# Performance work log

Measured on AMD Instinct MI355X. Metric: run time of the kernel, lower is better.

Reference implementation:

```python
import math
import jax, jax.numpy as jnp
import numpy as np

D_MODEL = 1024
N_HEADS = 16
D_K = D_MODEL // N_HEADS
THETA = 10000.0


def setup_inputs() -> dict:
    key = jax.random.key(0)
    k1, k2, k3 = jax.random.split(key, 3)
    B, S = 2, 2048
    x = jax.random.normal(k1, (B, S, D_MODEL), dtype=jnp.float32)
    std_qkv = math.sqrt(2.0 / (D_MODEL + 3 * D_MODEL))
    std_out = math.sqrt(2.0 / (D_MODEL + D_MODEL))
    # Linear weights stored as (out_features, in_features) to match the
    # einsum '... i, o i -> ... o' contraction (trunc-normal approximated
    # by clipped normal for the reference baseline).
    w_qkv = jnp.clip(jax.random.normal(k2, (3 * D_MODEL, D_MODEL), dtype=jnp.float32) * std_qkv,
                     -3 * std_qkv, 3 * std_qkv)
    b_qkv = jnp.zeros((3 * D_MODEL,), dtype=jnp.float32)
    w_out = jnp.clip(jax.random.normal(k3, (D_MODEL, D_MODEL), dtype=jnp.float32) * std_out,
                     -3 * std_out, 3 * std_out)
    b_out = jnp.zeros((D_MODEL,), dtype=jnp.float32)
    return {"x": x, "w_qkv": w_qkv, "b_qkv": b_qkv, "w_out": w_out, "b_out": b_out}


def _rope(t, cos, sin):
    # t: (B, H, S, D_K); cos/sin: (S, D_K//2) broadcast over batch/heads.
    B, H, S, d = t.shape
    tp = t.reshape(B, H, S, d // 2, 2)
    even, odd = tp[..., 0], tp[..., 1]
    r_even = even * cos - odd * sin
    r_odd = even * sin + odd * cos
    return jnp.stack([r_even, r_odd], axis=-1).reshape(B, H, S, d)


def reference(x, w_qkv, b_qkv, w_out, b_out):
    B, S, _ = x.shape
    # QKV projection: weight is (out, in)
    qkv = jnp.einsum('bsi,oi->bso', x, w_qkv) + b_qkv  # (B, S, 3*D_MODEL)
    qkv = qkv.reshape(B, S, 3, N_HEADS, D_K).transpose(2, 0, 3, 1, 4)  # (3, B, H, S, D_K)
    q, k, v = qkv[0], qkv[1], qkv[2]

    # RoPE with default token_positions = arange(S)
    inv_freq = THETA ** (-(jnp.arange(0, D_K, 2, dtype=jnp.float32)) / D_K)  # (D_K//2,)
    ang = jnp.arange(S, dtype=jnp.float32)[:, None] * inv_freq[None, :]      # (S, D_K//2)
    cos, sin = jnp.cos(ang), jnp.sin(ang)
    q = _rope(q, cos, sin)
    k = _rope(k, cos, sin)

    # Scaled dot-product attention in fp32 with causal mask
    scale = 1.0 / math.sqrt(D_K)
    scores = jnp.einsum('bhqd,bhkd->bhqk', q.astype(jnp.float32), k.astype(jnp.float32)) * scale
    causal = jnp.tril(jnp.ones((S, S), dtype=bool))
    scores = jnp.where(causal, scores, jnp.finfo(jnp.float32).min)
    # Custom softmax: exp(x - max) / (sum + 1e-8)
    ex = jnp.exp(scores - jnp.max(scores, axis=-1, keepdims=True))
    attn = ex / (jnp.sum(ex, axis=-1, keepdims=True) + 1e-8)
    attn = attn.astype(v.dtype)

    o = jnp.einsum('bhqk,bhkd->bhqd', attn, v)           # (B, H, S, D_K)
    o = o.transpose(0, 2, 1, 3).reshape(B, S, D_MODEL)    # (B, S, D_MODEL)
    out = jnp.einsum('bsi,oi->bso', o, w_out) + b_out
    return out
```

## Files before the change

kernel.cpp:

```cpp
#include <hip/hip_runtime.h>


typedef float f32x4 __attribute__((ext_vector_type(4)));
typedef float fvec4 __attribute__((ext_vector_type(4)));
typedef __bf16 bf16x8 __attribute__((ext_vector_type(8)));
typedef unsigned int u32x4 __attribute__((ext_vector_type(4)));

#define S_SZ 2048
#define NH 16
#define DK 64

static __device__ __forceinline__ unsigned short f2bf(float f) {
  unsigned int u = __builtin_bit_cast(unsigned int, f);
  u += 0x7fffu + ((u >> 16) & 1u);
  return (unsigned short)(u >> 16);
}
static __device__ __forceinline__ float bf2f(unsigned short h) {
  unsigned int u = ((unsigned int)h) << 16;
  return __builtin_bit_cast(float, u);
}
static __device__ __forceinline__ unsigned int pk2(float a, float b) {
  return (unsigned int)f2bf(a) | ((unsigned int)f2bf(b) << 16);
}
static __device__ __forceinline__ bf16x8 ld16g(const unsigned short* p) {
  return __builtin_bit_cast(bf16x8, *(const u32x4*)p);
}
static __device__ __forceinline__ void gload_lds16(const unsigned short* g,
                                                   unsigned short* l) {
  __builtin_amdgcn_global_load_lds(
      (const __attribute__((address_space(1))) void*)g,
      (__attribute__((address_space(3))) void*)l, 16, 0, 0);
}
static __device__ __forceinline__ float ex2(float x) {
  float r;
  asm("v_exp_f32 %0, %1" : "=v"(r) : "v"(x));
  return r;
}
static __device__ __forceinline__ unsigned int cvtpk(float a, float b) {
  unsigned int r;
  asm("v_cvt_pk_bf16_f32 %0, %1, %2" : "=v"(r) : "v"(a), "v"(b));
  return r;
}

template <int CTRL>
static __device__ __forceinline__ float dppmov(float x) {
  return __builtin_bit_cast(
      float, __builtin_amdgcn_update_dpp(0, __builtin_bit_cast(int, x), CTRL,
                                         0xF, 0xF, true));
}
static __device__ __forceinline__ float rmax16(float x) {
  x = fmaxf(x, dppmov<0xB1>(x));
  x = fmaxf(x, dppmov<0x4E>(x));
  x = fmaxf(x, dppmov<0x141>(x));
  x = fmaxf(x, dppmov<0x140>(x));
  return x;
}
static __device__ __forceinline__ float rsum16(float x) {
  x += dppmov<0xB1>(x);
  x += dppmov<0x4E>(x);
  x += dppmov<0x141>(x);
  x += dppmov<0x140>(x);
  return x;
}

__global__ __launch_bounds__(256) void cvt_bf16(
    const float* __restrict__ x, const float* __restrict__ wq,
    const float* __restrict__ wo, unsigned short* __restrict__ xb,
    unsigned short* __restrict__ wqb, unsigned short* __restrict__ wob) {
  const int u = blockIdx.x * 256 + threadIdx.x;
  const float* src;
  unsigned short* dst;
  int idx;
  if (u < 524288) { src = x; dst = xb; idx = u; }
  else if (u < 917504) { src = wq; dst = wqb; idx = u - 524288; }
  else { src = wo; dst = wob; idx = u - 917504; }
  const fvec4* p = (const fvec4*)(src + (size_t)idx * 8);
  const fvec4 f0 = p[0], f1 = p[1];
  u32x4 o;
  o[0] = pk2(f0[0], f0[1]); o[1] = pk2(f0[2], f0[3]);
  o[2] = pk2(f1[0], f1[1]); o[3] = pk2(f1[2], f1[3]);
  *(u32x4*)(dst + (size_t)idx * 8) = o;
}

template <bool OBF16>
__global__ __launch_bounds__(256) void gemm_bf16(
    const unsigned short* __restrict__ A, const unsigned short* __restrict__ B,
    const float* __restrict__ bias, void* __restrict__ Cp, int N, int K) {
  __shared__ unsigned short As[2][4096];
  __shared__ unsigned short Bs[2][4096];
  const int t = threadIdx.x;
  const int lane = t & 63, w = t >> 6;
  const int lo = lane & 15, g = lane >> 4;
  const int wr = (w >> 1) * 64, wc = (w & 1) * 64;
  const int gx = gridDim.x;
  int o = blockIdx.y * gx + blockIdx.x;
  const int nwg = gx * gridDim.y;
  o = (o & 7) * (nwg >> 3) + (o >> 3);
  const int by = o / gx, bx = o - by * gx;
  const int bRow = by * 128, bCol = bx * 128;
  const unsigned short* ap = A + (size_t)(bRow + (t >> 2)) * K + (t & 3) * 8;
  const unsigned short* bp = B + (size_t)(bCol + (t >> 2)) * K + (t & 3) * 8;
  const size_t rK = (size_t)64 * K;
  const int wb = w * 512;
  f32x4 acc[4][4] = {};
  gload_lds16(ap, As[0] + wb);
  gload_lds16(ap + rK, As[0] + 2048 + wb);
  gload_lds16(bp, Bs[0] + wb);
  gload_lds16(bp + rK, Bs[0] + 2048 + wb);
  const int nk = K >> 5;
  for (int kt = 0; kt < nk; ++kt) {
    __syncthreads();
    if (kt + 1 < nk) {
      const int k0 = (kt + 1) << 5;
      const int nb = (kt + 1) & 1;
      gload_lds16(ap + k0, As[nb] + wb);
      gload_lds16(ap + rK + k0, As[nb] + 2048 + wb);
      gload_lds16(bp + k0, Bs[nb] + wb);
      gload_lds16(bp + rK + k0, Bs[nb] + 2048 + wb);
    }
    const unsigned short* Ac = As[kt & 1];
    const unsigned short* Bc = Bs[kt & 1];
    bf16x8 aF[4], bF[4];
#pragma unroll
    for (int m = 0; m < 4; ++m) aF[m] = ld16g(Ac + (wr + m * 16 + lo) * 32 + 8 * g);
#pragma unroll
    for (int n = 0; n < 4; ++n) bF[n] = ld16g(Bc + (wc + n * 16 + lo) * 32 + 8 * g);
    __builtin_amdgcn_s_setprio(1);
#pragma unroll
    for (int m = 0; m < 4; ++m)
#pragma unroll
      for (int n = 0; n < 4; ++n)
        acc[m][n] = __builtin_amdgcn_mfma_f32_16x16x32_bf16(aF[m], bF[n], acc[m][n], 0, 0, 0);
    __builtin_amdgcn_s_setprio(0);
  }
#pragma unroll
  for (int m = 0; m < 4; ++m) {
#pragma unroll
    for (int n = 0; n < 4; ++n) {
      const int col = bCol + wc + n * 16 + lo;
      const float bv = bias[col];
#pragma unroll
      for (int r = 0; r < 4; ++r) {
        const int row = bRow + wr + m * 16 + g * 4 + r;
        const float v = acc[m][n][r] + bv;
        if constexpr (OBF16)
          ((unsigned short*)Cp)[(size_t)row * N + col] = f2bf(v);
        else
          ((float*)Cp)[(size_t)row * N + col] = v;
      }
    }
  }
}

__global__ __launch_bounds__(256) void rope_scatter(
    const unsigned short* __restrict__ qkv, unsigned short* __restrict__ Qo,
    unsigned short* __restrict__ Ko, unsigned short* __restrict__ Vt) {
  const int t = blockIdx.x * 256 + threadIdx.x;
  const int i = t & 31;
  const int s = (t >> 5) & (S_SZ - 1);
  const int h = (t >> 16) & (NH - 1);
  const int b = t >> 20;
  const unsigned short* row = qkv + (size_t)(b * S_SZ + s) * 3072;
  const float inv = exp2f((float)i * (-13.287712379549449f / 32.0f));
  const float ang = (float)s * inv;
  float sn, cs;
  sincosf(ang, &sn, &cs);
  const unsigned int qp = *(const unsigned int*)(row + h * 64 + 2 * i);
  const unsigned int kp = *(const unsigned int*)(row + 1024 + h * 64 + 2 * i);
  const unsigned int vp = *(const unsigned int*)(row + 2048 + h * 64 + 2 * i);
  const float qe = bf2f((unsigned short)qp), qo = bf2f((unsigned short)(qp >> 16));
  const float ke = bf2f((unsigned short)kp), ko = bf2f((unsigned short)(kp >> 16));
  const size_t hb = (size_t)(b * NH + h);
  const size_t qkbase = (hb * S_SZ + s) * DK + 2 * i;
  const float qs = 0.18033688011112042f;
  *(unsigned int*)(Qo + qkbase) =
      pk2((qe * cs - qo * sn) * qs, (qe * sn + qo * cs) * qs);
  *(unsigned int*)(Ko + qkbase) = pk2(ke * cs - ko * sn, ke * sn + ko * cs);
  const size_t vb = (hb * DK + 2 * i) * S_SZ + s;
  Vt[vb] = (unsigned short)vp;
  Vt[vb + S_SZ] = (unsigned short)(vp >> 16);
}

static __device__ __forceinline__ void stage8(const unsigned short* __restrict__ gbase,
                                              int gstride, unsigned short* tile, int t) {
  const int r = t >> 3;
  const int s16 = (t & 7) ^ (r & 7);
  gload_lds16(gbase + (size_t)r * gstride + (s16 << 3), tile + (t >> 6) * 512);
}

static __device__ __forceinline__ void attn_step(
    const unsigned short* __restrict__ Kl, const unsigned short* __restrict__ Vl,
    unsigned short* __restrict__ Pw, const bf16x8 aQ0, const bf16x8 aQ1,
    const bool diag, const int wq, const int lo, const int g,
    float* __restrict__ m, float* __restrict__ lsum, f32x4* __restrict__ oacc) {
  f32x4 s[4];
  __builtin_amdgcn_s_setprio(1);
#pragma unroll
  for (int c = 0; c < 4; ++c) {
    const int kr = c * 16 + lo;
    const int sw = kr & 7;
    const bf16x8 b0 =
        __builtin_bit_cast(bf16x8, *(const u32x4*)&Kl[kr * 64 + ((g ^ sw) << 3)]);
    const bf16x8 b1 =
        __builtin_bit_cast(bf16x8, *(const u32x4*)&Kl[kr * 64 + (((4 + g) ^ sw) << 3)]);
    f32x4 z = {};
    z = __builtin_amdgcn_mfma_f32_16x16x32_bf16(aQ0, b0, z, 0, 0, 0);
    z = __builtin_amdgcn_mfma_f32_16x16x32_bf16(aQ1, b1, z, 0, 0, 0);
    s[c] = z;
  }
  __builtin_amdgcn_s_setprio(0);
  if (diag) {
#pragma unroll
    for (int c = 0; c < 4; ++c)
#pragma unroll
      for (int r = 0; r < 4; ++r)
        if ((c * 16 + lo) > (wq * 16 + g * 4 + r)) s[c][r] = -__builtin_inff();
  }
  float rm[4];
#pragma unroll
  for (int r = 0; r < 4; ++r) {
    const float v = fmaxf(fmaxf(s[0][r], s[1][r]), fmaxf(s[2][r], s[3][r]));
    rm[r] = rmax16(v);
  }
  const bool grow = (rm[0] > m[0] + 8.f) | (rm[1] > m[1] + 8.f) |
                    (rm[2] > m[2] + 8.f) | (rm[3] > m[3] + 8.f);
  if (__any((int)grow)) {
#pragma unroll
    for (int r = 0; r < 4; ++r) {
      const float mn = fmaxf(m[r], rm[r]);
      const float alpha = ex2(m[r] - mn);
      m[r] = mn;
      lsum[r] *= alpha;
#pragma unroll
      for (int nt = 0; nt < 4; ++nt) oacc[nt][r] *= alpha;
    }
  }
#pragma unroll
  for (int r = 0; r < 4; ++r) {
    float rs = 0.f;
#pragma unroll
    for (int c = 0; c < 4; ++c) {
      const float p = ex2(s[c][r] - m[r]);
      s[c][r] = p;
      rs += p;
    }
    lsum[r] += rsum16(rs);
    const unsigned int u01 = cvtpk(s[0][r], s[1][r]);
    const unsigned int u23 = cvtpk(s[2][r], s[3][r]);
    unsigned short* pr = Pw + (g * 4 + r) * 72 + lo;
    pr[0] = (unsigned short)u01;
    pr[16] = (unsigned short)(u01 >> 16);
    pr[32] = (unsigned short)u23;
    pr[48] = (unsigned short)(u23 >> 16);
  }
  __builtin_amdgcn_s_setprio(1);
#pragma unroll
  for (int kc = 0; kc < 2; ++kc) {
    const bf16x8 aP =
        __builtin_bit_cast(bf16x8, *(const u32x4*)&Pw[lo * 72 + kc * 32 + 8 * g]);
#pragma unroll
    for (int nt = 0; nt < 4; ++nt) {
      const int d = nt * 16 + lo;
      const bf16x8 bV = __builtin_bit_cast(
          bf16x8, *(const u32x4*)&Vl[d * 64 + (((kc * 4 + g) ^ (d & 7)) << 3)]);
      oacc[nt] = __builtin_amdgcn_mfma_f32_16x16x32_bf16(aP, bV, oacc[nt], 0, 0, 0);
    }
  }
  __builtin_amdgcn_s_setprio(0);
}

__global__ __launch_bounds__(512, 2) void flash_attn(
    const unsigned short* __restrict__ Q, const unsigned short* __restrict__ K,
    const unsigned short* __restrict__ VT, unsigned short* __restrict__ O) {
  __shared__ unsigned short Kb[4][4096];
  __shared__ unsigned short Vb[4][4096];
  __shared__ unsigned short Pl[8][1152];
  const int t = threadIdx.x;
  const int lane = t & 63, w = t >> 6;
  const int lo = lane & 15, g = lane >> 4;
  const int flat = blockIdx.y * 16 + blockIdx.x;
  const int bh = ((flat & 7) << 2) | ((flat >> 3) & 3);
  const int j = flat >> 5;
  const int qa = j, qb = 31 - j;
  const unsigned short* Qh = Q + (size_t)bh * S_SZ * DK;
  const unsigned short* Kh = K + (size_t)bh * S_SZ * DK;
  const unsigned short* Vh = VT + (size_t)bh * DK * S_SZ;

  const int wq = w & 3;
  const bool s1 = w >= 4;
  const int rowMain = (s1 ? qb : qa) * 64 + wq * 16;
  const int rowB = qb * 64 + wq * 16;
  const bf16x8 aQ0 = ld16g(Qh + (size_t)(rowMain + lo) * DK + 8 * g);
  const bf16x8 aQ1 = ld16g(Qh + (size_t)(rowMain + lo) * DK + 32 + 8 * g);
  bf16x8 aQB0 = aQ0, aQB1 = aQ1;
  if (!s1) {
    aQB0 = ld16g(Qh + (size_t)(rowB + lo) * DK + 8 * g);
    aQB1 = ld16g(Qh + (size_t)(rowB + lo) * DK + 32 + 8 * g);
  }

  float mA[4], lA[4], mB[4], lB[4];
  f32x4 oA[4] = {}, oB[4] = {};
#pragma unroll
  for (int r = 0; r < 4; ++r) {
    mA[r] = mB[r] = -__builtin_inff();
    lA[r] = lB[r] = 0.f;
  }
  unsigned short* Pw = &Pl[w][0];

  stage8(Kh, DK, Kb[0], t);
  stage8(Vh, S_SZ, Vb[0], t);
  __syncthreads();
  for (int i = 0; i <= 16; ++i) {
    if (i < 15) {
      stage8(Kh + (size_t)(i + 1) * 64 * DK, DK, Kb[(i + 1) & 1], t);
      stage8(Vh + (i + 1) * 64, S_SZ, Vb[(i + 1) & 1], t);
    }
    if (i >= qa && i <= 15) {
      const int tile = 16 + (i - qa);
      stage8(Kh + (size_t)tile * 64 * DK, DK, Kb[2 + ((i - qa) & 1)], t);
      stage8(Vh + tile * 64, S_SZ, Vb[2 + ((i - qa) & 1)], t);
    }
    if (s1) {
      if (i < 16) {
        attn_step(Kb[i & 1], Vb[i & 1], Pw, aQ0, aQ1, false, wq, lo, g, mA, lA, oA);
      } else {
        float* ml = (float*)Pw;
#pragma unroll
        for (int r = 0; r < 4; ++r) {
          ml[r * 64 + lane] = mA[r];
          ml[(4 + r) * 64 + lane] = lA[r];
        }
        float* obase = (w < 6) ? ((float*)&Kb[1][0]) + (w - 4) * 1024
                               : ((float*)&Vb[1][0]) + (w - 6) * 1024;
#pragma unroll
        for (int nt = 0; nt < 4; ++nt)
#pragma unroll
          for (int r = 0; r < 4; ++r) obase[(nt * 4 + r) * 64 + lane] = oA[nt][r];
      }
    } else {
      if (i <= qa) {
        attn_step(Kb[i & 1], Vb[i & 1], Pw, aQ0, aQ1, i == qa, wq, lo, g, mA, lA, oA);
      } else {
        const int d = i - qa - 1;
        attn_step(Kb[2 + (d & 1)], Vb[2 + (d & 1)], Pw, aQB0, aQB1, i == 16, wq,
                  lo, g, mB, lB, oB);
      }
    }
    __syncthreads();
  }

  if (!s1) {
    const int b = bh >> 4, h = bh & 15;
#pragma unroll
    for (int r = 0; r < 4; ++r) {
      const float inv = 1.0f / (lA[r] + 1e-8f);
      const size_t base = ((size_t)(b * S_SZ + rowMain + g * 4 + r)) * 1024 + h * DK;
#pragma unroll
      for (int nt = 0; nt < 4; ++nt) O[base + nt * 16 + lo] = f2bf(oA[nt][r] * inv);
    }
    const float* ml = (const float*)&Pl[w + 4][0];
    const float* obase = (w < 2) ? ((const float*)&Kb[1][0]) + w * 1024
                                 : ((const float*)&Vb[1][0]) + (w - 2) * 1024;
#pragma unroll
    for (int r = 0; r < 4; ++r) {
      const float m1 = ml[r * 64 + lane], l1 = ml[(4 + r) * 64 + lane];
      const float mh = fmaxf(mB[r], m1);
      const float a0 = ex2(mB[r] - mh), a1 = ex2(m1 - mh);
      const float linv = 1.0f / (lB[r] * a0 + l1 * a1 + 1e-8f);
      const size_t base = ((size_t)(b * S_SZ + rowB + g * 4 + r)) * 1024 + h * DK;
#pragma unroll
      for (int nt = 0; nt < 4; ++nt)
        O[base + nt * 16 + lo] =
            f2bf((oB[nt][r] * a0 + obase[(nt * 4 + r) * 64 + lane] * a1) * linv);
    }
  }
}

extern "C" void kernel_launch(void* const* d_in, const int* in_sizes, int n_in,
                              void* d_out, int out_size, void* d_ws, size_t ws_size,
                              hipStream_t stream) {
  const float* x = (const float*)d_in[0];
  const float* w_qkv = (const float*)d_in[1];
  const float* b_qkv = (const float*)d_in[2];
  const float* w_out = (const float*)d_in[3];
  const float* b_out = (const float*)d_in[4];
  float* out = (float*)d_out;

  char* ws = (char*)d_ws;
  unsigned short* xb = (unsigned short*)(ws);
  unsigned short* wqb = (unsigned short*)(ws + 8388608);
  unsigned short* wob = (unsigned short*)(ws + 14680064);
  unsigned short* qkv = (unsigned short*)(ws + 16777216);
  unsigned short* kb = (unsigned short*)(ws + 41943040);
  unsigned short* vt = (unsigned short*)(ws + 50331648);
  unsigned short* qb = xb;
  unsigned short* ob = qkv;

  cvt_bf16<<<4096, 256, 0, stream>>>(x, w_qkv, w_out, xb, wqb, wob);
  {
    dim3 grid(3072 / 128, 4096 / 128);
    gemm_bf16<true><<<grid, 256, 0, stream>>>(xb, wqb, b_qkv, qkv, 3072, 1024);
  }
  rope_scatter<<<(2 * NH * S_SZ * 32) / 256, 256, 0, stream>>>(qkv, qb, kb, vt);
  {
    dim3 grid(16, 2 * NH);
    flash_attn<<<grid, 512, 0, stream>>>(qb, kb, vt, ob);
  }
  {
    dim3 grid(1024 / 128, 4096 / 128);
    gemm_bf16<false><<<grid, 256, 0, stream>>>(ob, wob, b_out, out, 1024, 1024);
  }
}
```

Measured before the change: 140.6 us.

## Read second-stream V directly from global memory and shrink LDS for higher occupancy

Drops the LDS staging buffers for the second query tile's V and has that path load V operands straight from global memory. It also repacks the per-wave P scratch from padded 72-stride rows into XOR-swizzled 64-stride rows. Together these cut shared memory use, and launch bounds are raised from 2 to 4 blocks per CU. The trade-off is uncached, uncoalesced-ish global loads inside the MFMA loop and possible register pressure at the higher occupancy target. The end-of-loop merge still writes into Vb[1], which the smaller buffer keeps.

```diff
diff --git a/kernel.cpp b/kernel.cpp
--- a/kernel.cpp
+++ b/kernel.cpp
@@ -188,8 +188,10 @@
   gload_lds16(gbase + (size_t)r * gstride + (s16 << 3), tile + (t >> 6) * 512);
 }
 
+template <bool VG>
 static __device__ __forceinline__ void attn_step(
     const unsigned short* __restrict__ Kl, const unsigned short* __restrict__ Vl,
+    const unsigned short* __restrict__ Vg, const int kb0,
     unsigned short* __restrict__ Pw, const bf16x8 aQ0, const bf16x8 aQ1,
     const bool diag, const int wq, const int lo, const int g,
     float* __restrict__ m, float* __restrict__ lsum, f32x4* __restrict__ oacc) {
@@ -247,34 +249,40 @@
     lsum[r] += rsum16(rs);
     const unsigned int u01 = cvtpk(s[0][r], s[1][r]);
     const unsigned int u23 = cvtpk(s[2][r], s[3][r]);
-    unsigned short* pr = Pw + (g * 4 + r) * 72 + lo;
-    pr[0] = (unsigned short)u01;
-    pr[16] = (unsigned short)(u01 >> 16);
-    pr[32] = (unsigned short)u23;
-    pr[48] = (unsigned short)(u23 >> 16);
+    const int prow = g * 4 + r;
+    const int rsw = prow & 7;
+    unsigned short* pr = Pw + prow * 64 + (lo & 7);
+    pr[(((lo >> 3) + 0) ^ rsw) << 3] = (unsigned short)u01;
+    pr[(((lo >> 3) + 2) ^ rsw) << 3] = (unsigned short)(u01 >> 16);
+    pr[(((lo >> 3) + 4) ^ rsw) << 3] = (unsigned short)u23;
+    pr[(((lo >> 3) + 6) ^ rsw) << 3] = (unsigned short)(u23 >> 16);
   }
   __builtin_amdgcn_s_setprio(1);
 #pragma unroll
   for (int kc = 0; kc < 2; ++kc) {
-    const bf16x8 aP =
-        __builtin_bit_cast(bf16x8, *(const u32x4*)&Pw[lo * 72 + kc * 32 + 8 * g]);
+    const bf16x8 aP = __builtin_bit_cast(
+        bf16x8, *(const u32x4*)&Pw[lo * 64 + (((kc * 4 + g) ^ (lo & 7)) << 3)]);
 #pragma unroll
     for (int nt = 0; nt < 4; ++nt) {
       const int d = nt * 16 + lo;
-      const bf16x8 bV = __builtin_bit_cast(
-          bf16x8, *(const u32x4*)&Vl[d * 64 + (((kc * 4 + g) ^ (d & 7)) << 3)]);
+      bf16x8 bV;
+      if constexpr (VG)
+        bV = ld16g(Vg + (size_t)d * S_SZ + kb0 + kc * 32 + 8 * g);
+      else
+        bV = __builtin_bit_cast(
+            bf16x8, *(const u32x4*)&Vl[d * 64 + (((kc * 4 + g) ^ (d & 7)) << 3)]);
       oacc[nt] = __builtin_amdgcn_mfma_f32_16x16x32_bf16(aP, bV, oacc[nt], 0, 0, 0);
     }
   }
   __builtin_amdgcn_s_setprio(0);
 }
 
-__global__ __launch_bounds__(512, 2) void flash_attn(
+__global__ __launch_bounds__(512, 4) void flash_attn(
     const unsigned short* __restrict__ Q, const unsigned short* __restrict__ K,
     const unsigned short* __restrict__ VT, unsigned short* __restrict__ O) {
   __shared__ unsigned short Kb[4][4096];
-  __shared__ unsigned short Vb[4][4096];
-  __shared__ unsigned short Pl[8][1152];
+  __shared__ unsigned short Vb[2][4096];
+  __shared__ unsigned short Pl[8][1024];
   const int t = threadIdx.x;
   const int lane = t & 63, w = t >> 6;
   const int lo = lane & 15, g = lane >> 4;
@@ -318,11 +326,11 @@
     if (i >= qa && i <= 15) {
       const int tile = 16 + (i - qa);
       stage8(Kh + (size_t)tile * 64 * DK, DK, Kb[2 + ((i - qa) & 1)], t);
-      stage8(Vh + tile * 64, S_SZ, Vb[2 + ((i - qa) & 1)], t);
     }
     if (s1) {
       if (i < 16) {
-        attn_step(Kb[i & 1], Vb[i & 1], Pw, aQ0, aQ1, false, wq, lo, g, mA, lA, oA);
+        attn_step<false>(Kb[i & 1], Vb[i & 1], nullptr, 0, Pw, aQ0, aQ1, false,
+                         wq, lo, g, mA, lA, oA);
       } else {
         float* ml = (float*)Pw;
 #pragma unroll
@@ -339,11 +347,13 @@
       }
     } else {
       if (i <= qa) {
-        attn_step(Kb[i & 1], Vb[i & 1], Pw, aQ0, aQ1, i == qa, wq, lo, g, mA, lA, oA);
+        attn_step<false>(Kb[i & 1], Vb[i & 1], nullptr, 0, Pw, aQ0, aQ1,
+                         i == qa, wq, lo, g, mA, lA, oA);
       } else {
         const int d = i - qa - 1;
-        attn_step(Kb[2 + (d & 1)], Vb[2 + (d & 1)], Pw, aQB0, aQB1, i == 16, wq,
-                  lo, g, mB, lB, oB);
+        const int tile = 16 + d;
+        attn_step<true>(Kb[2 + (d & 1)], nullptr, Vh, tile * 64, Pw, aQB0, aQB1,
+                        i == 16, wq, lo, g, mB, lB, oB);
       }
     }
     __syncthreads();
```

Measured after the change: 212.3 us. 1.51x slower.
